# Kernel optimization log

Hardware: AMD Instinct MI355X
Metric: run time of the kernel (lower is better)

## Reference

```python
import jax, jax.numpy as jnp
import numpy as np

N = 50000   # nodes
E = 800000  # edges
D = 128     # input = hidden = output dim
G = 64      # graphs in batch


def setup_inputs() -> dict:
    key = jax.random.key(0)
    ks = jax.random.split(key, 12)
    s = 1.0 / np.sqrt(D)
    x = jax.random.normal(ks[0], (N, D), dtype=jnp.float32)
    edge_index = jax.random.randint(ks[1], (2, E), 0, N, dtype=jnp.int64)
    batch = jnp.sort(jax.random.randint(ks[2], (N,), 0, G, dtype=jnp.int64))
    return {
        "x": x,
        "W1": jax.random.normal(ks[3], (D, D), jnp.float32) * s,
        "b1": jnp.zeros((D,), jnp.float32),
        "W2": jax.random.normal(ks[4], (D, D), jnp.float32) * s,
        "b2": jnp.zeros((D,), jnp.float32),
        "W3": jax.random.normal(ks[5], (D, D), jnp.float32) * s,
        "b3": jnp.zeros((D,), jnp.float32),
        "Wm1": jax.random.normal(ks[6], (D, D), jnp.float32) * s,
        "bm1": jnp.zeros((D,), jnp.float32),
        "Wm2": jax.random.normal(ks[7], (D, D), jnp.float32) * s,
        "bm2": jnp.zeros((D,), jnp.float32),
        "edge_index": edge_index,
        "batch": batch,
    }


def _gcn_conv(x, W, b, src, dst, deg_isqrt, num_nodes):
    # PyG GCNConv: h = D^{-1/2}(A+I)D^{-1/2} X W + b  (self-loops included in src/dst)
    h = x @ W  # [N, Dout]
    norm = deg_isqrt[src] * deg_isqrt[dst]  # [E+N]
    msg = h[src] * norm[:, None]            # gather + scale
    out = jax.ops.segment_sum(msg, dst, num_segments=num_nodes)  # scatter-add
    return out + b


def reference(x, W1, b1, W2, b2, W3, b3, Wm1, bm1, Wm2, bm2, edge_index, batch):
    num_nodes = x.shape[0]
    loop = jnp.arange(num_nodes, dtype=edge_index.dtype)
    src = jnp.concatenate([edge_index[0], loop])  # add self-loops
    dst = jnp.concatenate([edge_index[1], loop])
    # degree with self-loops (edge_weight = 1), computed on target nodes
    deg = jax.ops.segment_sum(jnp.ones_like(dst, dtype=x.dtype), dst,
                              num_segments=num_nodes)
    deg_isqrt = jnp.where(deg > 0, jax.lax.rsqrt(deg), 0.0)

    h = jax.nn.relu(_gcn_conv(x, W1, b1, src, dst, deg_isqrt, num_nodes))
    h = jax.nn.relu(_gcn_conv(h, W2, b2, src, dst, deg_isqrt, num_nodes))
    h = _gcn_conv(h, W3, b3, src, dst, deg_isqrt, num_nodes)

    # global_mean_pool over graph ids
    sums = jax.ops.segment_sum(h, batch, num_segments=G)
    cnts = jax.ops.segment_sum(jnp.ones((num_nodes,), h.dtype), batch,
                               num_segments=G)
    pooled = sums / jnp.maximum(cnts, 1.0)[:, None]  # [G, D]

    out = jax.nn.relu(pooled @ Wm1 + bm1) @ Wm2 + bm2
    return out
```

## Files before the change

kernel.cpp:

```cpp
#include <hip/hip_runtime.h>
#include <hip/hip_bf16.h>

typedef __attribute__((ext_vector_type(8))) short short8;
typedef __attribute__((ext_vector_type(4))) float floatx4;

#define SLAB_CAP 96

static __device__ __forceinline__ ushort f2b(float f) {
    __hip_bfloat16 h = __float2bfloat16(f);
    return __builtin_bit_cast(ushort, h);
}
static __device__ __forceinline__ float blo(uint u) {
    return __builtin_bit_cast(float, u << 16);
}
static __device__ __forceinline__ float bhi(uint u) {
    return __builtin_bit_cast(float, u & 0xffff0000u);
}
static __device__ __forceinline__ float b2f(ushort u) {
    return __builtin_bit_cast(float, (uint)u << 16);
}
static __device__ __forceinline__ uint pack2(float lo, float hi) {
    return (uint)f2b(lo) | ((uint)f2b(hi) << 16);
}

__global__ __launch_bounds__(256) void k_slab_fill(const int* __restrict__ src,
                                                   const int* __restrict__ dst, int E,
                                                   int* __restrict__ deg_cnt,
                                                   int* __restrict__ slab) {
    int e0 = (blockIdx.x * 256 + threadIdx.x) * 4;
    if (e0 + 3 < E) {
        int4 s = *(const int4*)(src + e0);
        int4 d = *(const int4*)(dst + e0);
        int p0 = atomicAdd(&deg_cnt[d.x], 1);
        int p1 = atomicAdd(&deg_cnt[d.y], 1);
        int p2 = atomicAdd(&deg_cnt[d.z], 1);
        int p3 = atomicAdd(&deg_cnt[d.w], 1);
        if (p0 < SLAB_CAP) slab[d.x * SLAB_CAP + p0] = s.x;
        if (p1 < SLAB_CAP) slab[d.y * SLAB_CAP + p1] = s.y;
        if (p2 < SLAB_CAP) slab[d.z * SLAB_CAP + p2] = s.z;
        if (p3 < SLAB_CAP) slab[d.w * SLAB_CAP + p3] = s.w;
    } else {
        for (int e = e0; e < E; ++e) {
            int d = dst[e];
            int p = atomicAdd(&deg_cnt[d], 1);
            if (p < SLAB_CAP) slab[d * SLAB_CAP + p] = src[e];
        }
    }
}

__global__ __launch_bounds__(256) void k_di_scale(const int* __restrict__ deg_cnt,
                                                  const uint* __restrict__ Hin,
                                                  uint* __restrict__ Hout,
                                                  float* __restrict__ di, int N) {
    int idx = blockIdx.x * 256 + threadIdx.x;
    int n = idx >> 6;
    int l = idx & 63;
    if (n >= N) return;
    float din = rsqrtf((float)(deg_cnt[n] + 1));
    if (l == 0) di[n] = din;
    uint u = Hin[(size_t)n * 64 + l];
    Hout[(size_t)n * 64 + l] = pack2(blo(u) * din, bhi(u) * din);
}

template <typename XT, int SCALE>
__global__ __launch_bounds__(256) void k_matmul_mfma(const XT* __restrict__ X,
                                                     const float* __restrict__ W,
                                                     const float* __restrict__ di,
                                                     ushort* __restrict__ Y,
                                                     int N, int tiles) {
    __shared__ ushort wt[128 * 128];
    int t = threadIdx.x;
    {
        int c0 = (t & 31) * 4;
        int k0 = (t >> 5) * 4;
#pragma unroll
        for (int i = 0; i < 4; i++) {
            int kk = k0 + i * 32;
            float4 r0 = *(const float4*)&W[(kk + 0) * 128 + c0];
            float4 r1 = *(const float4*)&W[(kk + 1) * 128 + c0];
            float4 r2 = *(const float4*)&W[(kk + 2) * 128 + c0];
            float4 r3 = *(const float4*)&W[(kk + 3) * 128 + c0];
            float colv[4][4] = {{r0.x, r1.x, r2.x, r3.x},
                                {r0.y, r1.y, r2.y, r3.y},
                                {r0.z, r1.z, r2.z, r3.z},
                                {r0.w, r1.w, r2.w, r3.w}};
#pragma unroll
            for (int j = 0; j < 4; j++) {
                int c = c0 + j;
                int chs = (kk >> 3) ^ (c & 7);
                int idx = c * 128 + (chs << 3) + (kk & 7);
                ushort4 v;
                v.x = f2b(colv[j][0]); v.y = f2b(colv[j][1]);
                v.z = f2b(colv[j][2]); v.w = f2b(colv[j][3]);
                *(ushort4*)&wt[idx] = v;
            }
        }
    }
    __syncthreads();
    int wv = t >> 6;
    int l  = t & 63;
    int lr = l & 15;
    int lk = l >> 4;
    for (int tile = blockIdx.x; tile < tiles; tile += gridDim.x) {
        int row = tile * 64 + wv * 16 + lr;
        int rowc = row < N ? row : N - 1;
        short8 a[4];
#pragma unroll
        for (int ks = 0; ks < 4; ks++) {
            int kb = lk * 8 + ks * 32;
            if constexpr (sizeof(XT) == 4) {
                const float* p = (const float*)X + (size_t)rowc * 128 + kb;
                float4 f0 = *(const float4*)p;
                float4 f1 = *(const float4*)(p + 4);
                short8 av;
                av[0] = (short)f2b(f0.x); av[1] = (short)f2b(f0.y);
                av[2] = (short)f2b(f0.z); av[3] = (short)f2b(f0.w);
                av[4] = (short)f2b(f1.x); av[5] = (short)f2b(f1.y);
                av[6] = (short)f2b(f1.z); av[7] = (short)f2b(f1.w);
                a[ks] = av;
            } else {
                a[ks] = *(const short8*)((const ushort*)X + (size_t)rowc * 128 + kb);
            }
        }
        floatx4 acc[8];
#pragma unroll
        for (int ct = 0; ct < 8; ct++) acc[ct] = (floatx4)(0.f);
#pragma unroll
        for (int ct = 0; ct < 8; ct++) {
            int col = ct * 16 + lr;
#pragma unroll
            for (int ks = 0; ks < 4; ks++) {
                int kb = lk * 8 + ks * 32;
                int chs = (kb >> 3) ^ (col & 7);
                short8 b = *(const short8*)&wt[col * 128 + (chs << 3)];
                acc[ct] = __builtin_amdgcn_mfma_f32_16x16x32_bf16(a[ks], b, acc[ct], 0, 0, 0);
            }
        }
        int rbase = tile * 64 + wv * 16 + lk * 4;
        float dr[4] = {1.f, 1.f, 1.f, 1.f};
        if constexpr (SCALE) {
            if (rbase + 3 < N) {
                float4 d4 = *(const float4*)&di[rbase];
                dr[0] = d4.x; dr[1] = d4.y; dr[2] = d4.z; dr[3] = d4.w;
            } else {
                dr[0] = rbase + 0 < N ? di[rbase + 0] : 0.f;
                dr[1] = rbase + 1 < N ? di[rbase + 1] : 0.f;
                dr[2] = rbase + 2 < N ? di[rbase + 2] : 0.f;
                dr[3] = rbase + 3 < N ? di[rbase + 3] : 0.f;
            }
        }
#pragma unroll
        for (int ct = 0; ct < 8; ct++) {
#pragma unroll
            for (int r = 0; r < 4; r++) {
                int ro = rbase + r;
                if (ro < N) Y[(size_t)ro * 128 + ct * 16 + lr] = f2b(acc[ct][r] * dr[r]);
            }
        }
    }
}

template <int RELU>
__global__ __launch_bounds__(256) void k_aggregate(const uint* __restrict__ H,
                                                   const float* __restrict__ di,
                                                   const int* __restrict__ deg_cnt,
                                                   const int* __restrict__ slab,
                                                   const float* __restrict__ bias,
                                                   uint* __restrict__ Y, int N) {
    int t = threadIdx.x;
    int node = blockIdx.x * 4 + (t >> 6);
    if (node >= N) return;
    int lane = t & 63;
    float din = di[node];
    uint hv = H[(size_t)node * 64 + lane];
    float ax = blo(hv), ay = bhi(hv);
    int deg = deg_cnt[node];
    if (deg > SLAB_CAP) deg = SLAB_CAP;
    const int* row = slab + (size_t)node * SLAB_CAP;
    int e = 0;
    for (; e + 3 < deg; e += 4) {
        int s0 = row[e], s1 = row[e + 1], s2 = row[e + 2], s3 = row[e + 3];
        uint g0 = H[(size_t)s0 * 64 + lane];
        uint g1 = H[(size_t)s1 * 64 + lane];
        uint g2 = H[(size_t)s2 * 64 + lane];
        uint g3 = H[(size_t)s3 * 64 + lane];
        ax += blo(g0) + blo(g1) + blo(g2) + blo(g3);
        ay += bhi(g0) + bhi(g1) + bhi(g2) + bhi(g3);
    }
    for (; e < deg; ++e) {
        uint g = H[(size_t)row[e] * 64 + lane];
        ax += blo(g); ay += bhi(g);
    }
    float2 b = *(const float2*)&bias[lane * 2];
    ax = ax * din + b.x; ay = ay * din + b.y;
    if (RELU) { ax = fmaxf(ax, 0.f); ay = fmaxf(ay, 0.f); }
    Y[(size_t)node * 64 + lane] = pack2(ax, ay);
}

__global__ __launch_bounds__(128) void k_pool(const ushort* __restrict__ H,
                                              const int* __restrict__ batch,
                                              float* __restrict__ sums, int N) {
    int d = threadIdx.x;
    int n0 = blockIdx.x * 64;
    int n1 = n0 + 64; if (n1 > N) n1 = N;
    if (n0 >= N) return;
    float acc = 0.f;
    int g = batch[n0];
    for (int n = n0; n < n1; ++n) {
        int gn = batch[n];
        if (gn != g) { atomicAdd(&sums[g * 128 + d], acc); acc = 0.f; g = gn; }
        acc += b2f(H[(size_t)n * 128 + d]);
    }
    atomicAdd(&sums[g * 128 + d], acc);
}

__global__ __launch_bounds__(128) void k_mlp(const float* __restrict__ sums,
                                             const int* __restrict__ batch, int N,
                                             const float* __restrict__ Wm1,
                                             const float* __restrict__ bm1,
                                             const float* __restrict__ Wm2,
                                             const float* __restrict__ bm2,
                                             float* __restrict__ out) {
    __shared__ float p[128], t1[128];
    int g = blockIdx.x, j = threadIdx.x;
    int n0, n1;
    {
        int lo = 0, hi = N;
        while (lo < hi) { int m = (lo + hi) >> 1; if (batch[m] < g) lo = m + 1; else hi = m; }
        n0 = lo;
        hi = N;
        while (lo < hi) { int m = (lo + hi) >> 1; if (batch[m] < g + 1) lo = m + 1; else hi = m; }
        n1 = lo;
    }
    float cnt = (float)(n1 - n0);
    p[j] = sums[g * 128 + j] / fmaxf(cnt, 1.0f);
    __syncthreads();
    float acc = bm1[j];
#pragma unroll 4
    for (int k = 0; k < 128; k++) acc += p[k] * Wm1[k * 128 + j];
    t1[j] = fmaxf(acc, 0.f);
    __syncthreads();
    float acc2 = bm2[j];
#pragma unroll 4
    for (int k = 0; k < 128; k++) acc2 += t1[k] * Wm2[k * 128 + j];
    out[g * 128 + j] = acc2;
}

extern "C" void kernel_launch(void* const* d_in, const int* in_sizes, int n_in,
                              void* d_out, int out_size, void* d_ws, size_t ws_size,
                              hipStream_t stream) {
    const float* x   = (const float*)d_in[0];
    const float* W1  = (const float*)d_in[1];
    const float* b1  = (const float*)d_in[2];
    const float* W2  = (const float*)d_in[3];
    const float* b2  = (const float*)d_in[4];
    const float* W3  = (const float*)d_in[5];
    const float* b3  = (const float*)d_in[6];
    const float* Wm1 = (const float*)d_in[7];
    const float* bm1 = (const float*)d_in[8];
    const float* Wm2 = (const float*)d_in[9];
    const float* bm2 = (const float*)d_in[10];
    const int* edge  = (const int*)d_in[11];
    const int* batch = (const int*)d_in[12];

    int N = in_sizes[0] / 128;
    int E = in_sizes[11] / 2;
    int G = out_size / 128;
    const int* esrc = edge;
    const int* edst = edge + E;

    char* w = (char*)d_ws;
    auto alloc = [&](size_t bytes) -> char* {
        char* p = w;
        w += (bytes + 255) & ~size_t(255);
        return p;
    };
    ushort* Hb     = (ushort*)alloc((size_t)N * 128 * 2);
    ushort* Gb     = (ushort*)alloc((size_t)N * 128 * 2);
    float*  di     = (float*)alloc((size_t)N * 4);
    int*    slab   = (int*)alloc((size_t)N * SLAB_CAP * 4);
    char*  zbase   = w;
    int*   deg_cnt = (int*)alloc((size_t)N * 4);
    float* psums   = (float*)alloc((size_t)G * 128 * 4);
    size_t zbytes  = (size_t)(w - zbase);

    hipMemsetAsync(zbase, 0, zbytes, stream);

    k_slab_fill<<<(E + 1023) / 1024, 256, 0, stream>>>(esrc, edst, E, deg_cnt, slab);

    int tiles64 = (N + 63) / 64;
    int mmgrid = tiles64 < 512 ? tiles64 : 512;

    k_matmul_mfma<float, 0><<<mmgrid, 256, 0, stream>>>(x, W1, nullptr, Gb, N, tiles64);
    k_di_scale<<<(N * 64 + 255) / 256, 256, 0, stream>>>(deg_cnt, (const uint*)Gb, (uint*)Hb, di, N);
    k_aggregate<1><<<(N + 3) / 4, 256, 0, stream>>>((const uint*)Hb, di, deg_cnt, slab, b1, (uint*)Gb, N);
    k_matmul_mfma<ushort, 1><<<mmgrid, 256, 0, stream>>>(Gb, W2, di, Hb, N, tiles64);
    k_aggregate<1><<<(N + 3) / 4, 256, 0, stream>>>((const uint*)Hb, di, deg_cnt, slab, b2, (uint*)Gb, N);
    k_matmul_mfma<ushort, 1><<<mmgrid, 256, 0, stream>>>(Gb, W3, di, Hb, N, tiles64);
    k_aggregate<0><<<(N + 3) / 4, 256, 0, stream>>>((const uint*)Hb, di, deg_cnt, slab, b3, (uint*)Gb, N);

    k_pool<<<(N + 63) / 64, 128, 0, stream>>>(Gb, batch, psums, N);
    k_mlp<<<G, 128, 0, stream>>>(psums, batch, N, Wm1, bm1, Wm2, bm2, (float*)d_out);
}
```

Before: 354.7 us.

## Fuse slab fill with first matmul and widen aggregate gather unroll

Merges the edge slab-fill kernel and the first-layer matmul into one launch, with block ranges split by role, so the atomic-bound fill and the MFMA matmul can run concurrently and one launch is dropped. Separately, the aggregate loop now loads neighbor indices as int4 and gathers eight rows per iteration into two independent accumulator pairs, raising memory-level parallelism. The fused kernel reserves 32KB of LDS even for fill blocks, which may limit how many of them are resident at once.

```diff
diff --git a/kernel.cpp b/kernel.cpp
--- a/kernel.cpp
+++ b/kernel.cpp
@@ -23,11 +23,11 @@
     return (uint)f2b(lo) | ((uint)f2b(hi) << 16);
 }
 
-__global__ __launch_bounds__(256) void k_slab_fill(const int* __restrict__ src,
-                                                   const int* __restrict__ dst, int E,
-                                                   int* __restrict__ deg_cnt,
-                                                   int* __restrict__ slab) {
-    int e0 = (blockIdx.x * 256 + threadIdx.x) * 4;
+static __device__ __forceinline__ void fill_body(int bid, const int* __restrict__ src,
+                                                 const int* __restrict__ dst, int E,
+                                                 int* __restrict__ deg_cnt,
+                                                 int* __restrict__ slab) {
+    int e0 = (bid * 256 + threadIdx.x) * 4;
     if (e0 + 3 < E) {
         int4 s = *(const int4*)(src + e0);
         int4 d = *(const int4*)(dst + e0);
@@ -48,27 +48,13 @@
     }
 }
 
-__global__ __launch_bounds__(256) void k_di_scale(const int* __restrict__ deg_cnt,
-                                                  const uint* __restrict__ Hin,
-                                                  uint* __restrict__ Hout,
-                                                  float* __restrict__ di, int N) {
-    int idx = blockIdx.x * 256 + threadIdx.x;
-    int n = idx >> 6;
-    int l = idx & 63;
-    if (n >= N) return;
-    float din = rsqrtf((float)(deg_cnt[n] + 1));
-    if (l == 0) di[n] = din;
-    uint u = Hin[(size_t)n * 64 + l];
-    Hout[(size_t)n * 64 + l] = pack2(blo(u) * din, bhi(u) * din);
-}
-
 template <typename XT, int SCALE>
-__global__ __launch_bounds__(256) void k_matmul_mfma(const XT* __restrict__ X,
-                                                     const float* __restrict__ W,
-                                                     const float* __restrict__ di,
-                                                     ushort* __restrict__ Y,
-                                                     int N, int tiles) {
-    __shared__ ushort wt[128 * 128];
+static __device__ __forceinline__ void mm_body(ushort* __restrict__ wt,
+                                               const XT* __restrict__ X,
+                                               const float* __restrict__ W,
+                                               const float* __restrict__ di,
+                                               ushort* __restrict__ Y,
+                                               int N, int tiles, int tile0, int tstride) {
     int t = threadIdx.x;
     {
         int c0 = (t & 31) * 4;
@@ -101,7 +87,7 @@
     int l  = t & 63;
     int lr = l & 15;
     int lk = l >> 4;
-    for (int tile = blockIdx.x; tile < tiles; tile += gridDim.x) {
+    for (int tile = tile0; tile < tiles; tile += tstride) {
         int row = tile * 64 + wv * 16 + lr;
         int rowc = row < N ? row : N - 1;
         short8 a[4];
@@ -160,6 +146,47 @@
     }
 }
 
+__global__ __launch_bounds__(256) void k_fill_mm(const int* __restrict__ src,
+                                                 const int* __restrict__ dst, int E,
+                                                 int* __restrict__ deg_cnt,
+                                                 int* __restrict__ slab,
+                                                 const float* __restrict__ X,
+                                                 const float* __restrict__ W,
+                                                 ushort* __restrict__ Y,
+                                                 int N, int tiles, int fillBlocks) {
+    __shared__ ushort wt[128 * 128];
+    int bid = blockIdx.x;
+    if (bid < fillBlocks) {
+        fill_body(bid, src, dst, E, deg_cnt, slab);
+        return;
+    }
+    mm_body<float, 0>(wt, X, W, nullptr, Y, N, tiles, bid - fillBlocks, gridDim.x - fillBlocks);
+}
+
+template <typename XT, int SCALE>
+__global__ __launch_bounds__(256) void k_matmul_mfma(const XT* __restrict__ X,
+                                                     const float* __restrict__ W,
+                                                     const float* __restrict__ di,
+                                                     ushort* __restrict__ Y,
+                                                     int N, int tiles) {
+    __shared__ ushort wt[128 * 128];
+    mm_body<XT, SCALE>(wt, X, W, di, Y, N, tiles, blockIdx.x, gridDim.x);
+}
+
+__global__ __launch_bounds__(256) void k_di_scale(const int* __restrict__ deg_cnt,
+                                                  const uint* __restrict__ Hin,
+                                                  uint* __restrict__ Hout,
+                                                  float* __restrict__ di, int N) {
+    int idx = blockIdx.x * 256 + threadIdx.x;
+    int n = idx >> 6;
+    int l = idx & 63;
+    if (n >= N) return;
+    float din = rsqrtf((float)(deg_cnt[n] + 1));
+    if (l == 0) di[n] = din;
+    uint u = Hin[(size_t)n * 64 + l];
+    Hout[(size_t)n * 64 + l] = pack2(blo(u) * din, bhi(u) * din);
+}
+
 template <int RELU>
 __global__ __launch_bounds__(256) void k_aggregate(const uint* __restrict__ H,
                                                    const float* __restrict__ di,
@@ -174,16 +201,33 @@
     float din = di[node];
     uint hv = H[(size_t)node * 64 + lane];
     float ax = blo(hv), ay = bhi(hv);
+    float bx = 0.f, by = 0.f;
     int deg = deg_cnt[node];
     if (deg > SLAB_CAP) deg = SLAB_CAP;
     const int* row = slab + (size_t)node * SLAB_CAP;
     int e = 0;
+    for (; e + 7 < deg; e += 8) {
+        int4 i0 = *(const int4*)(row + e);
+        int4 i1 = *(const int4*)(row + e + 4);
+        uint g0 = H[(size_t)i0.x * 64 + lane];
+        uint g1 = H[(size_t)i0.y * 64 + lane];
+        uint g2 = H[(size_t)i0.z * 64 + lane];
+        uint g3 = H[(size_t)i0.w * 64 + lane];
+        uint g4 = H[(size_t)i1.x * 64 + lane];
+        uint g5 = H[(size_t)i1.y * 64 + lane];
+        uint g6 = H[(size_t)i1.z * 64 + lane];
+        uint g7 = H[(size_t)i1.w * 64 + lane];
+        ax += blo(g0) + blo(g1) + blo(g2) + blo(g3);
+        ay += bhi(g0) + bhi(g1) + bhi(g2) + bhi(g3);
+        bx += blo(g4) + blo(g5) + blo(g6) + blo(g7);
+        by += bhi(g4) + bhi(g5) + bhi(g6) + bhi(g7);
+    }
     for (; e + 3 < deg; e += 4) {
-        int s0 = row[e], s1 = row[e + 1], s2 = row[e + 2], s3 = row[e + 3];
-        uint g0 = H[(size_t)s0 * 64 + lane];
-        uint g1 = H[(size_t)s1 * 64 + lane];
-        uint g2 = H[(size_t)s2 * 64 + lane];
-        uint g3 = H[(size_t)s3 * 64 + lane];
+        int4 i0 = *(const int4*)(row + e);
+        uint g0 = H[(size_t)i0.x * 64 + lane];
+        uint g1 = H[(size_t)i0.y * 64 + lane];
+        uint g2 = H[(size_t)i0.z * 64 + lane];
+        uint g3 = H[(size_t)i0.w * 64 + lane];
         ax += blo(g0) + blo(g1) + blo(g2) + blo(g3);
         ay += bhi(g0) + bhi(g1) + bhi(g2) + bhi(g3);
     }
@@ -191,6 +235,7 @@
         uint g = H[(size_t)row[e] * 64 + lane];
         ax += blo(g); ay += bhi(g);
     }
+    ax += bx; ay += by;
     float2 b = *(const float2*)&bias[lane * 2];
     ax = ax * din + b.x; ay = ay * din + b.y;
     if (RELU) { ax = fmaxf(ax, 0.f); ay = fmaxf(ay, 0.f); }
@@ -286,12 +331,12 @@
 
     hipMemsetAsync(zbase, 0, zbytes, stream);
 
-    k_slab_fill<<<(E + 1023) / 1024, 256, 0, stream>>>(esrc, edst, E, deg_cnt, slab);
-
     int tiles64 = (N + 63) / 64;
     int mmgrid = tiles64 < 512 ? tiles64 : 512;
-
-    k_matmul_mfma<float, 0><<<mmgrid, 256, 0, stream>>>(x, W1, nullptr, Gb, N, tiles64);
+    int fillBlocks = (E + 1023) / 1024;
+
+    k_fill_mm<<<fillBlocks + mmgrid, 256, 0, stream>>>(esrc, edst, E, deg_cnt, slab,
+                                                       x, W1, Gb, N, tiles64, fillBlocks);
     k_di_scale<<<(N * 64 + 255) / 256, 256, 0, stream>>>(deg_cnt, (const uint*)Gb, (uint*)Hb, di, N);
     k_aggregate<1><<<(N + 3) / 4, 256, 0, stream>>>((const uint*)Hb, di, deg_cnt, slab, b1, (uint*)Gb, N);
     k_matmul_mfma<ushort, 1><<<mmgrid, 256, 0, stream>>>(Gb, W2, di, Hb, N, tiles64);
```

New measurement: 324.6 us. 1.09x faster.
